# Kernel tuning notes

Measured on AMD Instinct MI355X. Metric: run time of the kernel, lower is better.

Reference implementation:

```python
import jax, jax.numpy as jnp
import numpy as np

NUM_STATES = 32768
NUM_LABELS = 64
BATCH = 512


def setup_inputs() -> dict:
    key = jax.random.key(0)
    k1, k2, k3, k4 = jax.random.split(key, 4)
    f = jax.random.normal(k1, (BATCH, NUM_LABELS), dtype=jnp.float32)
    # legal_state: binary indicator matrix [num_states, num_labels]
    S = jax.random.randint(k2, (NUM_STATES, NUM_LABELS), 0, 2).astype(jnp.float32)
    y = jax.random.uniform(k3, (BATCH, NUM_LABELS), dtype=jnp.float32)
    mask = jax.random.randint(k4, (BATCH, NUM_LABELS), 0, 2).astype(jnp.float32)
    return {"f": f, "S": S, "y": y, "mask": mask}


def reference(f, S, y, mask):
    # potential[s, b] = sum_i S[s, i] * f[b, i]
    potential = jnp.einsum('si,bi->sb', S, f)
    # stable softmax over the state axis (replaces exp/max/sum in original)
    P = jax.nn.softmax(potential, axis=0)  # [num_states, batch]
    # pMargin[b, i] = sum_{s: S[s,i]>0} P[s, b]  ->  indicator-matrix GEMM
    pMargin = jnp.einsum('sb,si->bi', P, S)  # [batch, num_labels]
    # per-column BCE (torch BCELoss clamps log at -100), masked, mean over batch
    logp = jnp.clip(jnp.log(pMargin), -100.0, None)
    log1mp = jnp.clip(jnp.log(1.0 - pMargin), -100.0, None)
    bce = -(y * logp + (1.0 - y) * log1mp) * mask  # [batch, num_labels]
    loss = jnp.sum(jnp.mean(bce, axis=0))  # sum over columns of per-column means
    return loss, pMargin
```

## Files before the change

kernel.cpp:

```cpp
#include <hip/hip_runtime.h>
#include <hip/hip_bf16.h>
#include <math.h>

#define N_STATES 32768
#define N_LABELS 64
#define N_BATCH  512

#define WS_Z    64
#define WS_M    576
#define WS_U    1088
#define WS_FLOATS (WS_U + N_LABELS * N_BATCH)

#define LSTRIDE 72

typedef __attribute__((ext_vector_type(8))) short  bfrag;
typedef __attribute__((ext_vector_type(4))) float  f32x4;

static __device__ __forceinline__ unsigned short f2bf(float x) {
    __hip_bfloat16 h = __float2bfloat16(x);
    return *reinterpret_cast<unsigned short*>(&h);
}
static __device__ __forceinline__ float bf2f(unsigned short u) {
    __hip_bfloat16 h;
    *reinterpret_cast<unsigned short*>(&h) = u;
    return __bfloat162float(h);
}

__global__ void init_kernel(const float* __restrict__ f, float* __restrict__ ws,
                            float* __restrict__ out) {
    int idx = blockIdx.x * 256 + threadIdx.x;
    if (idx == 0) out[0] = 0.f;
    if (idx >= WS_FLOATS) return;
    if (idx >= WS_M && idx < WS_M + N_BATCH) {
        int b = idx - WS_M;
        const float* fr = f + b * N_LABELS;
        float m = 0.f;
        #pragma unroll
        for (int i = 0; i < N_LABELS; i++) m += fmaxf(fr[i], 0.f);
        ws[idx] = m;
    } else {
        ws[idx] = 0.f;
    }
}

__global__ __launch_bounds__(256, 2) void
fused_kernel(const float* __restrict__ f, const float* __restrict__ S,
             float* __restrict__ ws) {
    __shared__ alignas(16) unsigned short f_hi[64 * LSTRIDE];
    __shared__ alignas(16) unsigned short f_lo[64 * LSTRIDE];
    __shared__ alignas(16) unsigned short S_t [64 * LSTRIDE];
    __shared__ alignas(16) unsigned short ST_t[64 * LSTRIDE];
    __shared__ alignas(16) unsigned short E_hi[64 * LSTRIDE];
    __shared__ alignas(16) unsigned short E_lo[64 * LSTRIDE];

    float* Z = ws + WS_Z;
    const float* M = ws + WS_M;
    float* U = ws + WS_U;

    const int t     = threadIdx.x;
    const int lane  = t & 63;
    const int w     = t >> 6;
    const int x     = lane & 15;
    const int quad  = lane >> 4;
    const int btile = blockIdx.x & 7;
    const int chunk = blockIdx.x >> 3;

    {
        const int row = t >> 2;
        const int q   = t & 3;
        const float4* p = reinterpret_cast<const float4*>(
            f + (size_t)(btile * 64 + row) * N_LABELS + q * 16);
        float4 v[4] = {p[0], p[1], p[2], p[3]};
        const float* vf = reinterpret_cast<const float*>(v);
        #pragma unroll
        for (int j = 0; j < 16; j++) {
            float val = vf[j];
            unsigned short h = f2bf(val);
            f_hi[row * LSTRIDE + q * 16 + j] = h;
            f_lo[row * LSTRIDE + q * 16 + j] = f2bf(val - bf2f(h));
        }
    }

    f32x4 Uacc[4];
    #pragma unroll
    for (int nt = 0; nt < 4; nt++) Uacc[nt] = (f32x4){0.f, 0.f, 0.f, 0.f};
    float zacc[4] = {0.f, 0.f, 0.f, 0.f};
    float Mv[4];
    #pragma unroll
    for (int nt = 0; nt < 4; nt++) Mv[nt] = M[btile * 64 + nt * 16 + x];

    const int sbase = chunk * 512;
    for (int st = 0; st < 8; st++) {
        const int s0 = sbase + st * 64;
        __syncthreads();
        {
            const int row = t >> 2;
            const int q   = t & 3;
            const float4* p = reinterpret_cast<const float4*>(
                S + (size_t)(s0 + row) * N_LABELS + q * 16);
            float4 v[4] = {p[0], p[1], p[2], p[3]};
            const float* vf = reinterpret_cast<const float*>(v);
            #pragma unroll
            for (int j = 0; j < 16; j++) {
                unsigned short h = f2bf(vf[j]);
                S_t [row * LSTRIDE + q * 16 + j] = h;
                ST_t[(q * 16 + j) * LSTRIDE + row] = h;
            }
        }
        __syncthreads();

        bfrag a0 = *reinterpret_cast<const bfrag*>(&S_t[(16 * w + x) * LSTRIDE + quad * 8]);
        bfrag a1 = *reinterpret_cast<const bfrag*>(&S_t[(16 * w + x) * LSTRIDE + 32 + quad * 8]);
        #pragma unroll
        for (int nt = 0; nt < 4; nt++) {
            const int frow = (nt * 16 + x) * LSTRIDE + quad * 8;
            bfrag bh0 = *reinterpret_cast<const bfrag*>(&f_hi[frow]);
            bfrag bh1 = *reinterpret_cast<const bfrag*>(&f_hi[frow + 32]);
            bfrag bl0 = *reinterpret_cast<const bfrag*>(&f_lo[frow]);
            bfrag bl1 = *reinterpret_cast<const bfrag*>(&f_lo[frow + 32]);
            f32x4 acc = (f32x4){0.f, 0.f, 0.f, 0.f};
            acc = __builtin_amdgcn_mfma_f32_16x16x32_bf16(a0, bh0, acc, 0, 0, 0);
            acc = __builtin_amdgcn_mfma_f32_16x16x32_bf16(a1, bh1, acc, 0, 0, 0);
            acc = __builtin_amdgcn_mfma_f32_16x16x32_bf16(a0, bl0, acc, 0, 0, 0);
            acc = __builtin_amdgcn_mfma_f32_16x16x32_bf16(a1, bl1, acc, 0, 0, 0);

            ushort4 eh, el;
            float e0 = __expf(acc[0] - Mv[nt]);
            float e1 = __expf(acc[1] - Mv[nt]);
            float e2 = __expf(acc[2] - Mv[nt]);
            float e3 = __expf(acc[3] - Mv[nt]);
            zacc[nt] += (e0 + e1) + (e2 + e3);
            eh.x = f2bf(e0); el.x = f2bf(e0 - bf2f(eh.x));
            eh.y = f2bf(e1); el.y = f2bf(e1 - bf2f(eh.y));
            eh.z = f2bf(e2); el.z = f2bf(e2 - bf2f(eh.z));
            eh.w = f2bf(e3); el.w = f2bf(e3 - bf2f(eh.w));
            const int eoff = (nt * 16 + x) * LSTRIDE + 16 * w + quad * 4;
            *reinterpret_cast<ushort4*>(&E_hi[eoff]) = eh;
            *reinterpret_cast<ushort4*>(&E_lo[eoff]) = el;
        }
        __syncthreads();

        bfrag c0 = *reinterpret_cast<const bfrag*>(&ST_t[(16 * w + x) * LSTRIDE + quad * 8]);
        bfrag c1 = *reinterpret_cast<const bfrag*>(&ST_t[(16 * w + x) * LSTRIDE + 32 + quad * 8]);
        #pragma unroll
        for (int nt = 0; nt < 4; nt++) {
            const int erow = (nt * 16 + x) * LSTRIDE + quad * 8;
            bfrag eh0 = *reinterpret_cast<const bfrag*>(&E_hi[erow]);
            bfrag eh1 = *reinterpret_cast<const bfrag*>(&E_hi[erow + 32]);
            bfrag el0 = *reinterpret_cast<const bfrag*>(&E_lo[erow]);
            bfrag el1 = *reinterpret_cast<const bfrag*>(&E_lo[erow + 32]);
            Uacc[nt] = __builtin_amdgcn_mfma_f32_16x16x32_bf16(c0, eh0, Uacc[nt], 0, 0, 0);
            Uacc[nt] = __builtin_amdgcn_mfma_f32_16x16x32_bf16(c1, eh1, Uacc[nt], 0, 0, 0);
            Uacc[nt] = __builtin_amdgcn_mfma_f32_16x16x32_bf16(c0, el0, Uacc[nt], 0, 0, 0);
            Uacc[nt] = __builtin_amdgcn_mfma_f32_16x16x32_bf16(c1, el1, Uacc[nt], 0, 0, 0);
        }
    }

    #pragma unroll
    for (int nt = 0; nt < 4; nt++) {
        #pragma unroll
        for (int r = 0; r < 4; r++) {
            int i = 16 * w + quad * 4 + r;
            int b = btile * 64 + nt * 16 + x;
            atomicAdd(&U[i * N_BATCH + b], Uacc[nt][r]);
        }
    }
    #pragma unroll
    for (int nt = 0; nt < 4; nt++) {
        float v = zacc[nt];
        v += __shfl_down(v, 32, 64);
        v += __shfl_down(v, 16, 64);
        if (quad == 0)
            atomicAdd(&Z[btile * 64 + nt * 16 + x], v);
    }
}

__global__ void finalize_kernel(const float* __restrict__ ws,
                                const float* __restrict__ y,
                                const float* __restrict__ mask,
                                float* __restrict__ out) {
    const float* Z = ws + WS_Z;
    const float* U = ws + WS_U;

    int idx = blockIdx.x * 256 + threadIdx.x;
    int b = idx >> 6;
    int i = idx & 63;

    float p = U[i * N_BATCH + b] / Z[b];
    p = fminf(fmaxf(p, 0.f), 1.f);
    out[1 + idx] = p;

    float lp  = fmaxf(logf(p), -100.f);
    float l1p = fmaxf(logf(1.f - p), -100.f);
    float yy = y[idx];
    float bce = -(yy * lp + (1.f - yy) * l1p) * mask[idx] * (1.f / (float)N_BATCH);

    float v = bce;
    #pragma unroll
    for (int off = 32; off > 0; off >>= 1) v += __shfl_down(v, off, 64);
    __shared__ float wsum[4];
    if ((threadIdx.x & 63) == 0) wsum[threadIdx.x >> 6] = v;
    __syncthreads();
    if (threadIdx.x == 0)
        atomicAdd(&out[0], wsum[0] + wsum[1] + wsum[2] + wsum[3]);
}

extern "C" void kernel_launch(void* const* d_in, const int* in_sizes, int n_in,
                              void* d_out, int out_size, void* d_ws, size_t ws_size,
                              hipStream_t stream) {
    const float* f    = (const float*)d_in[0];
    const float* S    = (const float*)d_in[1];
    const float* y    = (const float*)d_in[2];
    const float* mask = (const float*)d_in[3];
    float* out = (float*)d_out;
    float* ws  = (float*)d_ws;

    init_kernel<<<(WS_FLOATS + 255) / 256, 256, 0, stream>>>(f, ws, out);
    fused_kernel<<<512, 256, 0, stream>>>(f, S, ws);
    finalize_kernel<<<(N_BATCH * N_LABELS) / 256, 256, 0, stream>>>(ws, y, mask, out);
}
```

Before: 103.2 us.

## Pre-convert S to swizzled bf16 and double-buffer tiles via direct global-to-LDS loads

Result: no change. 103.1 us (-0.2%).

```diff
diff --git a/kernel.cpp b/kernel.cpp
--- a/kernel.cpp
+++ b/kernel.cpp
@@ -9,12 +9,12 @@
 #define WS_Z    64
 #define WS_M    576
 #define WS_U    1088
-#define WS_FLOATS (WS_U + N_LABELS * N_BATCH)
-
-#define LSTRIDE 72
-
-typedef __attribute__((ext_vector_type(8))) short  bfrag;
-typedef __attribute__((ext_vector_type(4))) float  f32x4;
+#define SB_BYTE  262144u
+#define STB_BYTE (SB_BYTE + 4194304u)
+
+typedef __attribute__((ext_vector_type(8))) short          bfrag;
+typedef __attribute__((ext_vector_type(4))) float          f32x4;
+typedef __attribute__((ext_vector_type(8))) unsigned short u16x8;
 
 static __device__ __forceinline__ unsigned short f2bf(float x) {
     __hip_bfloat16 h = __float2bfloat16(x);
@@ -26,133 +26,184 @@
     return __bfloat162float(h);
 }
 
-__global__ void init_kernel(const float* __restrict__ f, float* __restrict__ ws,
-                            float* __restrict__ out) {
-    int idx = blockIdx.x * 256 + threadIdx.x;
-    if (idx == 0) out[0] = 0.f;
-    if (idx >= WS_FLOATS) return;
-    if (idx >= WS_M && idx < WS_M + N_BATCH) {
-        int b = idx - WS_M;
-        const float* fr = f + b * N_LABELS;
-        float m = 0.f;
-        #pragma unroll
-        for (int i = 0; i < N_LABELS; i++) m += fmaxf(fr[i], 0.f);
-        ws[idx] = m;
-    } else {
-        ws[idx] = 0.f;
-    }
-}
-
-__global__ __launch_bounds__(256, 2) void
-fused_kernel(const float* __restrict__ f, const float* __restrict__ S,
-             float* __restrict__ ws) {
-    __shared__ alignas(16) unsigned short f_hi[64 * LSTRIDE];
-    __shared__ alignas(16) unsigned short f_lo[64 * LSTRIDE];
-    __shared__ alignas(16) unsigned short S_t [64 * LSTRIDE];
-    __shared__ alignas(16) unsigned short ST_t[64 * LSTRIDE];
-    __shared__ alignas(16) unsigned short E_hi[64 * LSTRIDE];
-    __shared__ alignas(16) unsigned short E_lo[64 * LSTRIDE];
+typedef __attribute__((address_space(1))) const unsigned char g_u8;
+typedef __attribute__((address_space(3))) unsigned char       l_u8;
+static __device__ __forceinline__ void dma16(const void* g, void* l) {
+    __builtin_amdgcn_global_load_lds((g_u8*)g, (l_u8*)l, 16, 0, 0);
+}
+
+__global__ __launch_bounds__(256) void prep_kernel(
+    const float* __restrict__ f, const float* __restrict__ S,
+    float* __restrict__ ws, float* __restrict__ out) {
+    const int tb = blockIdx.x;
+    const int t  = threadIdx.x;
+
+    if (tb == 512) {
+        if (t == 0) out[0] = 0.f;
+        for (int b = t; b < N_BATCH; b += 256) {
+            ws[WS_Z + b] = 0.f;
+            const float* fr = f + b * N_LABELS;
+            float m = 0.f;
+            #pragma unroll
+            for (int i = 0; i < N_LABELS; i++) m += fmaxf(fr[i], 0.f);
+            ws[WS_M + b] = m;
+        }
+        return;
+    }
+
+    if (t < 64) ws[WS_U + tb * 64 + t] = 0.f;
+
+    __shared__ alignas(16) unsigned short Sl[64 * 72];
+
+    unsigned short* SbW = (unsigned short*)((char*)ws + SB_BYTE);
+    unsigned short* StW = (unsigned short*)((char*)ws + STB_BYTE);
+
+    const int r = t >> 2;
+    const int q = t & 3;
+    const int m = r & 7;
+
+    const float4* p4 = reinterpret_cast<const float4*>(
+        S + ((size_t)(tb * 64 + r)) * N_LABELS + q * 16);
+    float4 v0 = p4[0], v1 = p4[1], v2 = p4[2], v3 = p4[3];
+    float vf[16] = {v0.x,v0.y,v0.z,v0.w, v1.x,v1.y,v1.z,v1.w,
+                    v2.x,v2.y,v2.z,v2.w, v3.x,v3.y,v3.z,v3.w};
+    u16x8 lo8, hi8;
+    #pragma unroll
+    for (int j = 0; j < 8; j++) { lo8[j] = f2bf(vf[j]); hi8[j] = f2bf(vf[8 + j]); }
+
+    *(u16x8*)&Sl[r * 72 + q * 16]     = lo8;
+    *(u16x8*)&Sl[r * 72 + q * 16 + 8] = hi8;
+
+    {
+        unsigned short* dst = SbW + (size_t)tb * 4096 + r * 64 + (((2 * q) ^ (m & 6)) * 8);
+        if (m & 1) { *(u16x8*)dst = hi8; *(u16x8*)(dst + 8) = lo8; }
+        else       { *(u16x8*)dst = lo8; *(u16x8*)(dst + 8) = hi8; }
+    }
+    __syncthreads();
+
+    const int i  = r;
+    const int mi = i & 7;
+    u16x8 tlo, thi;
+    #pragma unroll
+    for (int j = 0; j < 8; j++) {
+        tlo[j] = Sl[(16 * q + j)     * 72 + i];
+        thi[j] = Sl[(16 * q + 8 + j) * 72 + i];
+    }
+    {
+        unsigned short* dst = StW + (size_t)tb * 4096 + i * 64 + (((2 * q) ^ (mi & 6)) * 8);
+        if (mi & 1) { *(u16x8*)dst = thi; *(u16x8*)(dst + 8) = tlo; }
+        else        { *(u16x8*)dst = tlo; *(u16x8*)(dst + 8) = thi; }
+    }
+}
+
+__global__ __launch_bounds__(256, 2) void fused_kernel(
+    const float* __restrict__ f, float* __restrict__ ws) {
+    __shared__ alignas(16) unsigned short Sb2[2][4096];
+    __shared__ alignas(16) unsigned short St2[2][4096];
+    __shared__ alignas(16) unsigned short Et[64 * 72];
 
     float* Z = ws + WS_Z;
     const float* M = ws + WS_M;
     float* U = ws + WS_U;
+    const char* SbG = (const char*)ws + SB_BYTE;
+    const char* StG = (const char*)ws + STB_BYTE;
 
     const int t     = threadIdx.x;
     const int lane  = t & 63;
     const int w     = t >> 6;
     const int x     = lane & 15;
     const int quad  = lane >> 4;
+    const int mm    = x & 7;
     const int btile = blockIdx.x & 7;
     const int chunk = blockIdx.x >> 3;
-
-    {
-        const int row = t >> 2;
-        const int q   = t & 3;
-        const float4* p = reinterpret_cast<const float4*>(
-            f + (size_t)(btile * 64 + row) * N_LABELS + q * 16);
-        float4 v[4] = {p[0], p[1], p[2], p[3]};
-        const float* vf = reinterpret_cast<const float*>(v);
-        #pragma unroll
-        for (int j = 0; j < 16; j++) {
-            float val = vf[j];
-            unsigned short h = f2bf(val);
-            f_hi[row * LSTRIDE + q * 16 + j] = h;
-            f_lo[row * LSTRIDE + q * 16 + j] = f2bf(val - bf2f(h));
-        }
-    }
+    const int tile0 = chunk * 8;
+
+    bfrag fh[4][2], fl[4][2];
+    #pragma unroll
+    for (int nt = 0; nt < 4; nt++) {
+        const float4* fp = reinterpret_cast<const float4*>(
+            f + ((size_t)(btile * 64 + nt * 16 + x)) * N_LABELS);
+        #pragma unroll
+        for (int kh = 0; kh < 2; kh++) {
+            float4 a = fp[kh * 8 + quad * 2];
+            float4 b = fp[kh * 8 + quad * 2 + 1];
+            float vv[8] = {a.x,a.y,a.z,a.w, b.x,b.y,b.z,b.w};
+            #pragma unroll
+            for (int j = 0; j < 8; j++) {
+                unsigned short h = f2bf(vv[j]);
+                fh[nt][kh][j] = (short)h;
+                fl[nt][kh][j] = (short)f2bf(vv[j] - bf2f(h));
+            }
+        }
+    }
+    float Mv[4];
+    #pragma unroll
+    for (int nt = 0; nt < 4; nt++) Mv[nt] = M[btile * 64 + nt * 16 + x];
 
     f32x4 Uacc[4];
     #pragma unroll
     for (int nt = 0; nt < 4; nt++) Uacc[nt] = (f32x4){0.f, 0.f, 0.f, 0.f};
     float zacc[4] = {0.f, 0.f, 0.f, 0.f};
-    float Mv[4];
-    #pragma unroll
-    for (int nt = 0; nt < 4; nt++) Mv[nt] = M[btile * 64 + nt * 16 + x];
-
-    const int sbase = chunk * 512;
+
+    auto stage = [&](int tile, int buf) {
+        size_t gb = (size_t)tile * 8192 + (size_t)w * 2048 + (size_t)lane * 16;
+        int lo = w * 2048;
+        dma16(SbG + gb,        (char*)&Sb2[buf][0] + lo);
+        dma16(SbG + gb + 1024, (char*)&Sb2[buf][0] + lo + 1024);
+        dma16(StG + gb,        (char*)&St2[buf][0] + lo);
+        dma16(StG + gb + 1024, (char*)&St2[buf][0] + lo + 1024);
+    };
+
+    stage(tile0 + 0, 0);
+    stage(tile0 + 1, 1);
+    asm volatile("s_waitcnt vmcnt(4)" ::: "memory");
+    asm volatile("s_barrier" ::: "memory");
+
+    #pragma unroll
     for (int st = 0; st < 8; st++) {
-        const int s0 = sbase + st * 64;
-        __syncthreads();
-        {
-            const int row = t >> 2;
-            const int q   = t & 3;
-            const float4* p = reinterpret_cast<const float4*>(
-                S + (size_t)(s0 + row) * N_LABELS + q * 16);
-            float4 v[4] = {p[0], p[1], p[2], p[3]};
-            const float* vf = reinterpret_cast<const float*>(v);
-            #pragma unroll
-            for (int j = 0; j < 16; j++) {
-                unsigned short h = f2bf(vf[j]);
-                S_t [row * LSTRIDE + q * 16 + j] = h;
-                ST_t[(q * 16 + j) * LSTRIDE + row] = h;
-            }
-        }
-        __syncthreads();
-
-        bfrag a0 = *reinterpret_cast<const bfrag*>(&S_t[(16 * w + x) * LSTRIDE + quad * 8]);
-        bfrag a1 = *reinterpret_cast<const bfrag*>(&S_t[(16 * w + x) * LSTRIDE + 32 + quad * 8]);
+        const int cur = st & 1;
+        const unsigned short* Sb = &Sb2[cur][0];
+        const unsigned short* St = &St2[cur][0];
+
+        bfrag a0 = *(const bfrag*)(Sb + (16 * w + x) * 64 + ((quad ^ mm) * 8));
+        bfrag a1 = *(const bfrag*)(Sb + (16 * w + x) * 64 + (((quad + 4) ^ mm) * 8));
         #pragma unroll
         for (int nt = 0; nt < 4; nt++) {
-            const int frow = (nt * 16 + x) * LSTRIDE + quad * 8;
-            bfrag bh0 = *reinterpret_cast<const bfrag*>(&f_hi[frow]);
-            bfrag bh1 = *reinterpret_cast<const bfrag*>(&f_hi[frow + 32]);
-            bfrag bl0 = *reinterpret_cast<const bfrag*>(&f_lo[frow]);
-            bfrag bl1 = *reinterpret_cast<const bfrag*>(&f_lo[frow + 32]);
             f32x4 acc = (f32x4){0.f, 0.f, 0.f, 0.f};
-            acc = __builtin_amdgcn_mfma_f32_16x16x32_bf16(a0, bh0, acc, 0, 0, 0);
-            acc = __builtin_amdgcn_mfma_f32_16x16x32_bf16(a1, bh1, acc, 0, 0, 0);
-            acc = __builtin_amdgcn_mfma_f32_16x16x32_bf16(a0, bl0, acc, 0, 0, 0);
-            acc = __builtin_amdgcn_mfma_f32_16x16x32_bf16(a1, bl1, acc, 0, 0, 0);
-
-            ushort4 eh, el;
+            acc = __builtin_amdgcn_mfma_f32_16x16x32_bf16(a0, fh[nt][0], acc, 0, 0, 0);
+            acc = __builtin_amdgcn_mfma_f32_16x16x32_bf16(a1, fh[nt][1], acc, 0, 0, 0);
+            acc = __builtin_amdgcn_mfma_f32_16x16x32_bf16(a0, fl[nt][0], acc, 0, 0, 0);
+            acc = __builtin_amdgcn_mfma_f32_16x16x32_bf16(a1, fl[nt][1], acc, 0, 0, 0);
             float e0 = __expf(acc[0] - Mv[nt]);
             float e1 = __expf(acc[1] - Mv[nt]);
             float e2 = __expf(acc[2] - Mv[nt]);
             float e3 = __expf(acc[3] - Mv[nt]);
             zacc[nt] += (e0 + e1) + (e2 + e3);
-            eh.x = f2bf(e0); el.x = f2bf(e0 - bf2f(eh.x));
-            eh.y = f2bf(e1); el.y = f2bf(e1 - bf2f(eh.y));
-            eh.z = f2bf(e2); el.z = f2bf(e2 - bf2f(eh.z));
-            eh.w = f2bf(e3); el.w = f2bf(e3 - bf2f(eh.w));
-            const int eoff = (nt * 16 + x) * LSTRIDE + 16 * w + quad * 4;
-            *reinterpret_cast<ushort4*>(&E_hi[eoff]) = eh;
-            *reinterpret_cast<ushort4*>(&E_lo[eoff]) = el;
-        }
-        __syncthreads();
-
-        bfrag c0 = *reinterpret_cast<const bfrag*>(&ST_t[(16 * w + x) * LSTRIDE + quad * 8]);
-        bfrag c1 = *reinterpret_cast<const bfrag*>(&ST_t[(16 * w + x) * LSTRIDE + 32 + quad * 8]);
+            ushort4 ev;
+            ev.x = f2bf(e0); ev.y = f2bf(e1); ev.z = f2bf(e2); ev.w = f2bf(e3);
+            *(ushort4*)&Et[(nt * 16 + x) * 72 + 16 * w + quad * 4] = ev;
+        }
+        asm volatile("s_waitcnt lgkmcnt(0)" ::: "memory");
+        asm volatile("s_barrier" ::: "memory");
+
+        bfrag c0 = *(const bfrag*)(St + (16 * w + x) * 64 + ((quad ^ mm) * 8));
+        bfrag c1 = *(const bfrag*)(St + (16 * w + x) * 64 + (((quad + 4) ^ mm) * 8));
         #pragma unroll
         for (int nt = 0; nt < 4; nt++) {
-            const int erow = (nt * 16 + x) * LSTRIDE + quad * 8;
-            bfrag eh0 = *reinterpret_cast<const bfrag*>(&E_hi[erow]);
-            bfrag eh1 = *reinterpret_cast<const bfrag*>(&E_hi[erow + 32]);
-            bfrag el0 = *reinterpret_cast<const bfrag*>(&E_lo[erow]);
-            bfrag el1 = *reinterpret_cast<const bfrag*>(&E_lo[erow + 32]);
-            Uacc[nt] = __builtin_amdgcn_mfma_f32_16x16x32_bf16(c0, eh0, Uacc[nt], 0, 0, 0);
-            Uacc[nt] = __builtin_amdgcn_mfma_f32_16x16x32_bf16(c1, eh1, Uacc[nt], 0, 0, 0);
-            Uacc[nt] = __builtin_amdgcn_mfma_f32_16x16x32_bf16(c0, el0, Uacc[nt], 0, 0, 0);
-            Uacc[nt] = __builtin_amdgcn_mfma_f32_16x16x32_bf16(c1, el1, Uacc[nt], 0, 0, 0);
+            bfrag e0 = *(const bfrag*)(Et + (nt * 16 + x) * 72 + quad * 8);
+            bfrag e1 = *(const bfrag*)(Et + (nt * 16 + x) * 72 + 32 + quad * 8);
+            Uacc[nt] = __builtin_amdgcn_mfma_f32_16x16x32_bf16(c0, e0, Uacc[nt], 0, 0, 0);
+            Uacc[nt] = __builtin_amdgcn_mfma_f32_16x16x32_bf16(c1, e1, Uacc[nt], 0, 0, 0);
+        }
+
+        if (st < 6) {
+            asm volatile("s_barrier" ::: "memory");
+            stage(tile0 + st + 2, cur);
+            asm volatile("s_waitcnt vmcnt(4)" ::: "memory");
+            asm volatile("s_barrier" ::: "memory");
+        } else if (st == 6) {
+            asm volatile("s_waitcnt vmcnt(0)" ::: "memory");
+            asm volatile("s_barrier" ::: "memory");
         }
     }
 
@@ -170,8 +221,7 @@
         float v = zacc[nt];
         v += __shfl_down(v, 32, 64);
         v += __shfl_down(v, 16, 64);
-        if (quad == 0)
-            atomicAdd(&Z[btile * 64 + nt * 16 + x], v);
+        if (quad == 0) atomicAdd(&Z[btile * 64 + nt * 16 + x], v);
     }
 }
 
@@ -215,7 +265,7 @@
     float* out = (float*)d_out;
     float* ws  = (float*)d_ws;
 
-    init_kernel<<<(WS_FLOATS + 255) / 256, 256, 0, stream>>>(f, ws, out);
-    fused_kernel<<<512, 256, 0, stream>>>(f, S, ws);
-    finalize_kernel<<<(N_BATCH * N_LABELS) / 256, 256, 0, stream>>>(ws, y, mask, out);
-}
+    prep_kernel<<<513, 256, 0, stream>>>(f, S, ws, out);
+    fused_kernel<<<512, 256, 0, stream>>>(f, ws);
+    finalize_kernel<<<128, 256, 0, stream>>>(ws, y, mask, out);
+}
```
